# Performance work log

Hardware: AMD Instinct MI355X
Metric: run time of the kernel (lower is better)

## Reference

```python
import jax, jax.numpy as jnp
import numpy as np

WIN_LEN = 400
HOP = 100
NFFT = 512


def _make_kernel():
    # rfft of identity -> DFT basis, truncated to window length
    fb = np.fft.rfft(np.eye(NFFT))[:WIN_LEN]          # [WIN_LEN, NFFT//2+1] complex
    kernel = np.concatenate([fb.real, fb.imag], axis=1).T  # [2*(NFFT//2+1), WIN_LEN]
    # periodic (fftbins=True) Hamming window, as scipy.signal.get_window('hamming', N, fftbins=True)
    n = np.arange(WIN_LEN)
    window = (0.54 - 0.46 * np.cos(2.0 * np.pi * n / WIN_LEN)).astype(np.float32)
    kernel = kernel.astype(np.float32)[:, None, :] * window  # [514, 1, WIN_LEN]
    return jnp.asarray(kernel)


def setup_inputs() -> dict:
    key = jax.random.key(0)
    x = jax.random.normal(key, (32, 480000), dtype=jnp.float32)  # [B, T] raw audio
    return {"x": x, "weight": _make_kernel()}


def reference(x, weight):
    # x: [B, T] -> [B, 1, T]; pad both sides by (window_len - hop)
    pad = WIN_LEN - HOP
    xp = jnp.pad(x[:, None, :], ((0, 0), (0, 0), (pad, pad)))
    # strided conv against fixed Fourier basis -> [B, 2*(NFFT//2+1), n_frames]
    out = jax.lax.conv_general_dilated(
        xp, weight,
        window_strides=(HOP,),
        padding='VALID',
        dimension_numbers=('NCH', 'OIH', 'NCH'),
    )
    return out
```

## Files before the change

kernel.cpp:

```cpp
#include <hip/hip_runtime.h>
#include <hip/hip_bf16.h>


#define T_LEN   480000
#define NF      4803
#define C_OUT   514
#define HOP     100
#define WIN     400
#define BM      128
#define BN      64
#define WSTR    424
#define XPS     487040
#define XP_TOTAL (32 * XPS)
#define WP_ROWS 576
#define WP_ELEMS (WP_ROWS * WSTR)
#define WP_BYTE_OFF ((size_t)XP_TOTAL * 2)
#define WS_NEEDED (WP_BYTE_OFF + (size_t)WP_ELEMS * 2)
#define MT_CNT  38
#define NT_CNT  9
#define XSEG    13312

typedef __attribute__((ext_vector_type(8))) short short8;
typedef __attribute__((ext_vector_type(4))) float f32x4;

__device__ __forceinline__ unsigned short f2bf(float f) {
    unsigned int u = __float_as_uint(f);
    u += 0x7FFFu + ((u >> 16) & 1u);
    return (unsigned short)(u >> 16);
}

__device__ __forceinline__ void gl_lds16(const unsigned short* g, unsigned short* l) {
    __builtin_amdgcn_global_load_lds(
        (const __attribute__((address_space(1))) unsigned int*)(g),
        (__attribute__((address_space(3))) unsigned int*)(l), 16, 0, 0);
}

__global__ void cvt_x_kernel(const float* __restrict__ x, unsigned short* __restrict__ xp) {
    const int t = blockIdx.x * 256 + threadIdx.x;
    const int b  = t / (XPS / 4);
    const int i4 = t - b * (XPS / 4);
    const int i  = i4 * 4;
    const int g  = i - 300;
    ushort4 h;
    if (g >= 0 && g + 3 < T_LEN) {
        const float4 f = *(const float4*)(x + (size_t)b * T_LEN + g);
        h.x = f2bf(f.x); h.y = f2bf(f.y); h.z = f2bf(f.z); h.w = f2bf(f.w);
    } else {
        const float* xb = x + (size_t)b * T_LEN;
        h.x = (g + 0 >= 0 && g + 0 < T_LEN) ? f2bf(xb[g + 0]) : 0;
        h.y = (g + 1 >= 0 && g + 1 < T_LEN) ? f2bf(xb[g + 1]) : 0;
        h.z = (g + 2 >= 0 && g + 2 < T_LEN) ? f2bf(xb[g + 2]) : 0;
        h.w = (g + 3 >= 0 && g + 3 < T_LEN) ? f2bf(xb[g + 3]) : 0;
    }
    *(ushort4*)(xp + (size_t)b * XPS + i) = h;
}

__global__ void cvt_w_kernel(const float* __restrict__ w, unsigned short* __restrict__ wp) {
    const int t = blockIdx.x * 256 + threadIdx.x;
    if (t >= WP_ELEMS) return;
    const int c = t / WSTR;
    const int k = t - c * WSTR;
    wp[t] = (c < C_OUT && k < WIN) ? f2bf(w[(size_t)c * WIN + k]) : 0;
}

__global__ __launch_bounds__(256, 2)
void stft_gemm(const unsigned short* __restrict__ xp,
               const unsigned short* __restrict__ wp,
               float* __restrict__ out) {
    __shared__ unsigned short x_s[XSEG];
    __shared__ unsigned short w_s[BN * WSTR];

    const int tid  = threadIdx.x;
    const int lane = tid & 63;
    const int wv   = tid >> 6;
    const int nt   = blockIdx.x;
    const int mt   = blockIdx.y;
    const int b    = blockIdx.z;

    const unsigned short* xg = xp + (size_t)b * XPS + mt * (BM * HOP);
    #pragma unroll
    for (int c = wv; c < 26; c += 4) {
        const int idx = (c << 6) + lane;
        gl_lds16(xg + idx * 8, x_s + idx * 8);
    }
    const unsigned short* wg = wp + (size_t)nt * (BN * WSTR);
    #pragma unroll
    for (int c = wv; c < 53; c += 4) {
        const int idx = (c << 6) + lane;
        gl_lds16(wg + idx * 8, w_s + idx * 8);
    }
    __syncthreads();

    const int q  = lane >> 4;
    const int lm = lane & 15;

    f32x4 acc[2][4];
    #pragma unroll
    for (int mi = 0; mi < 2; ++mi)
        #pragma unroll
        for (int ni = 0; ni < 4; ++ni)
            acc[mi][ni] = (f32x4){0.f, 0.f, 0.f, 0.f};

    const int a0 = (wv * 32 + lm) * HOP + q * 8;
    const int a1 = a0 + 16 * HOP;
    int boff[4];
    #pragma unroll
    for (int ni = 0; ni < 4; ++ni) boff[ni] = (ni * 16 + lm) * WSTR + q * 8;

    #pragma unroll
    for (int kc = 0; kc < 13; ++kc) {
        const int k = kc * 32;
        union { short8 v; unsigned long long u[2]; } au0, au1;
        {
            const unsigned long long* p0 = (const unsigned long long*)(x_s + a0 + k);
            const unsigned long long* p1 = (const unsigned long long*)(x_s + a1 + k);
            au0.u[0] = p0[0]; au0.u[1] = p0[1];
            au1.u[0] = p1[0]; au1.u[1] = p1[1];
        }
        #pragma unroll
        for (int ni = 0; ni < 4; ++ni) {
            const short8 bf = *(const short8*)(&w_s[boff[ni] + k]);
            acc[0][ni] = __builtin_amdgcn_mfma_f32_16x16x32_bf16(au0.v, bf, acc[0][ni], 0, 0, 0);
            acc[1][ni] = __builtin_amdgcn_mfma_f32_16x16x32_bf16(au1.v, bf, acc[1][ni], 0, 0, 0);
        }
    }

    float* ob = out + (size_t)b * C_OUT * NF;
    const int f_base = mt * BM + wv * 32 + q * 4;
    const int c_base = nt * BN + lm;
    #pragma unroll
    for (int mi = 0; mi < 2; ++mi) {
        const int fg = f_base + mi * 16;
        const bool fok = (fg + 3 < NF);
        #pragma unroll
        for (int ni = 0; ni < 4; ++ni) {
            const int cg = c_base + ni * 16;
            if (cg < C_OUT) {
                float* op = ob + (size_t)cg * NF + fg;
                if (fok) {
                    op[0] = acc[mi][ni][0]; op[1] = acc[mi][ni][1];
                    op[2] = acc[mi][ni][2]; op[3] = acc[mi][ni][3];
                } else {
                    #pragma unroll
                    for (int r = 0; r < 4; ++r)
                        if (fg + r < NF) op[r] = acc[mi][ni][r];
                }
            }
        }
    }
}

#define SEG 13120
__global__ __launch_bounds__(256, 2)
void conv_stft_fallback(const float* __restrict__ x,
                        const float* __restrict__ w,
                        float* __restrict__ out) {
    __shared__ short x_s[SEG];
    __shared__ short w_s[BN * WSTR];
    const int tid = threadIdx.x;
    const int nt  = blockIdx.x;
    const int mt  = blockIdx.y;
    const int b   = blockIdx.z;
    const int s0 = mt * (BM * HOP) - 300;
    const float* xb = x + (size_t)b * T_LEN;
    for (int v = tid; v < SEG / 4; v += 256) {
        int g = s0 + v * 4;
        float f0, f1, f2, f3;
        if (g >= 0 && g + 3 < T_LEN) {
            const float4 f = *(const float4*)(xb + g);
            f0 = f.x; f1 = f.y; f2 = f.z; f3 = f.w;
        } else {
            f0 = (g + 0 >= 0 && g + 0 < T_LEN) ? xb[g + 0] : 0.f;
            f1 = (g + 1 >= 0 && g + 1 < T_LEN) ? xb[g + 1] : 0.f;
            f2 = (g + 2 >= 0 && g + 2 < T_LEN) ? xb[g + 2] : 0.f;
            f3 = (g + 3 >= 0 && g + 3 < T_LEN) ? xb[g + 3] : 0.f;
        }
        ushort4 h; h.x = f2bf(f0); h.y = f2bf(f1); h.z = f2bf(f2); h.w = f2bf(f3);
        *(ushort4*)(&x_s[v * 4]) = h;
    }
    for (int s = tid; s < BN * 106; s += 256) {
        const int r  = s / 106;
        const int gk = s - r * 106;
        const int c  = nt * BN + r;
        ushort4 h = make_ushort4(0, 0, 0, 0);
        if (gk < 100 && c < C_OUT) {
            const float4 f = *(const float4*)(w + (size_t)c * WIN + gk * 4);
            h.x = f2bf(f.x); h.y = f2bf(f.y); h.z = f2bf(f.z); h.w = f2bf(f.w);
        }
        if (gk * 4 < WSTR) *(ushort4*)(&w_s[r * WSTR + gk * 4]) = h;
    }
    __syncthreads();
    const int lane = tid & 63, wv = tid >> 6, q = lane >> 4, lm = lane & 15;
    f32x4 acc[2][4];
    #pragma unroll
    for (int mi = 0; mi < 2; ++mi)
        #pragma unroll
        for (int ni = 0; ni < 4; ++ni) acc[mi][ni] = (f32x4){0.f,0.f,0.f,0.f};
    const int a0 = (wv * 32 + lm) * HOP + q * 8;
    const int a1 = a0 + 16 * HOP;
    int boff[4];
    #pragma unroll
    for (int ni = 0; ni < 4; ++ni) boff[ni] = (ni * 16 + lm) * WSTR + q * 8;
    #pragma unroll
    for (int kc = 0; kc < 13; ++kc) {
        const int k = kc * 32;
        union { short8 v; unsigned long long u[2]; } au0, au1;
        const unsigned long long* p0 = (const unsigned long long*)(x_s + a0 + k);
        const unsigned long long* p1 = (const unsigned long long*)(x_s + a1 + k);
        au0.u[0] = p0[0]; au0.u[1] = p0[1];
        au1.u[0] = p1[0]; au1.u[1] = p1[1];
        #pragma unroll
        for (int ni = 0; ni < 4; ++ni) {
            const short8 bf = *(const short8*)(&w_s[boff[ni] + k]);
            acc[0][ni] = __builtin_amdgcn_mfma_f32_16x16x32_bf16(au0.v, bf, acc[0][ni], 0, 0, 0);
            acc[1][ni] = __builtin_amdgcn_mfma_f32_16x16x32_bf16(au1.v, bf, acc[1][ni], 0, 0, 0);
        }
    }
    float* ob = out + (size_t)b * C_OUT * NF;
    const int f_base = mt * BM + wv * 32 + q * 4;
    const int c_base = nt * BN + lm;
    #pragma unroll
    for (int mi = 0; mi < 2; ++mi) {
        #pragma unroll
        for (int ni = 0; ni < 4; ++ni) {
            const int cg = c_base + ni * 16;
            if (cg < C_OUT) {
                float* op = ob + (size_t)cg * NF;
                #pragma unroll
                for (int r = 0; r < 4; ++r) {
                    const int fg = f_base + mi * 16 + r;
                    if (fg < NF) op[fg] = acc[mi][ni][r];
                }
            }
        }
    }
}

extern "C" void kernel_launch(void* const* d_in, const int* in_sizes, int n_in,
                              void* d_out, int out_size, void* d_ws, size_t ws_size,
                              hipStream_t stream) {
    const float* x = (const float*)d_in[0];
    const float* w = (const float*)d_in[1];
    float* out = (float*)d_out;

    if (ws_size >= WS_NEEDED) {
        unsigned short* xp = (unsigned short*)d_ws;
        unsigned short* wp = (unsigned short*)((char*)d_ws + WP_BYTE_OFF);
        cvt_x_kernel<<<XP_TOTAL / 4 / 256, 256, 0, stream>>>(x, xp);
        cvt_w_kernel<<<(WP_ELEMS + 255) / 256, 256, 0, stream>>>(w, wp);
        dim3 grid(NT_CNT, MT_CNT, 32);
        stft_gemm<<<grid, 256, 0, stream>>>(xp, wp, out);
    } else {
        dim3 grid(NT_CNT, MT_CNT, 32);
        conv_stft_fallback<<<grid, 256, 0, stream>>>(x, w, out);
    }
}
```

Baseline: 455.9 us.

## Use 2-wave blocks with 4x4 MFMA tiles and XCD-aware block remapping

Halves the block to 128 threads, so each wave now computes a 64x64 output tile (4x4 MFMA fragments) instead of 32x64. This raises register-level reuse of A and B fragments read from LDS. The 3D grid is flattened to 1D and remapped so consecutive logical tiles land on the same XCD, aiming for better L2 locality of shared x and weight segments. The cost is more accumulator registers per thread and fewer waves per block to hide the global-to-LDS loads.

Measured after the change: 461.5 us. No clear change (+1.2%).

```diff
diff --git a/kernel.cpp b/kernel.cpp
--- a/kernel.cpp
+++ b/kernel.cpp
@@ -18,6 +18,8 @@
 #define WS_NEEDED (WP_BYTE_OFF + (size_t)WP_ELEMS * 2)
 #define MT_CNT  38
 #define NT_CNT  9
+#define TOT_BLK (NT_CNT * MT_CNT * 32)
+#define XCD_CHUNK (TOT_BLK / 8)
 #define XSEG    13312
 
 typedef __attribute__((ext_vector_type(8))) short short8;
@@ -63,7 +65,7 @@
     wp[t] = (c < C_OUT && k < WIN) ? f2bf(w[(size_t)c * WIN + k]) : 0;
 }
 
-__global__ __launch_bounds__(256, 2)
+__global__ __launch_bounds__(128, 2)
 void stft_gemm(const unsigned short* __restrict__ xp,
                const unsigned short* __restrict__ wp,
                float* __restrict__ out) {
@@ -73,19 +75,23 @@
     const int tid  = threadIdx.x;
     const int lane = tid & 63;
     const int wv   = tid >> 6;
-    const int nt   = blockIdx.x;
-    const int mt   = blockIdx.y;
-    const int b    = blockIdx.z;
+
+    const int id  = blockIdx.x;
+    const int lid = (id & 7) * XCD_CHUNK + (id >> 3);
+    const int nt  = lid % NT_CNT;
+    const int r1  = lid / NT_CNT;
+    const int mt  = r1 % MT_CNT;
+    const int b   = r1 / MT_CNT;
 
     const unsigned short* xg = xp + (size_t)b * XPS + mt * (BM * HOP);
     #pragma unroll
-    for (int c = wv; c < 26; c += 4) {
+    for (int c = wv; c < 26; c += 2) {
         const int idx = (c << 6) + lane;
         gl_lds16(xg + idx * 8, x_s + idx * 8);
     }
     const unsigned short* wg = wp + (size_t)nt * (BN * WSTR);
     #pragma unroll
-    for (int c = wv; c < 53; c += 4) {
+    for (int c = wv; c < 53; c += 2) {
         const int idx = (c << 6) + lane;
         gl_lds16(wg + idx * 8, w_s + idx * 8);
     }
@@ -94,15 +100,16 @@
     const int q  = lane >> 4;
     const int lm = lane & 15;
 
-    f32x4 acc[2][4];
-    #pragma unroll
-    for (int mi = 0; mi < 2; ++mi)
+    f32x4 acc[4][4];
+    #pragma unroll
+    for (int mi = 0; mi < 4; ++mi)
         #pragma unroll
         for (int ni = 0; ni < 4; ++ni)
             acc[mi][ni] = (f32x4){0.f, 0.f, 0.f, 0.f};
 
-    const int a0 = (wv * 32 + lm) * HOP + q * 8;
-    const int a1 = a0 + 16 * HOP;
+    int aoff[4];
+    #pragma unroll
+    for (int mi = 0; mi < 4; ++mi) aoff[mi] = (wv * 64 + mi * 16 + lm) * HOP + q * 8;
     int boff[4];
     #pragma unroll
     for (int ni = 0; ni < 4; ++ni) boff[ni] = (ni * 16 + lm) * WSTR + q * 8;
@@ -110,26 +117,26 @@
     #pragma unroll
     for (int kc = 0; kc < 13; ++kc) {
         const int k = kc * 32;
-        union { short8 v; unsigned long long u[2]; } au0, au1;
-        {
-            const unsigned long long* p0 = (const unsigned long long*)(x_s + a0 + k);
-            const unsigned long long* p1 = (const unsigned long long*)(x_s + a1 + k);
-            au0.u[0] = p0[0]; au0.u[1] = p0[1];
-            au1.u[0] = p1[0]; au1.u[1] = p1[1];
+        union { short8 v; unsigned long long u[2]; } au[4];
+        #pragma unroll
+        for (int mi = 0; mi < 4; ++mi) {
+            const unsigned long long* p = (const unsigned long long*)(x_s + aoff[mi] + k);
+            au[mi].u[0] = p[0]; au[mi].u[1] = p[1];
         }
         #pragma unroll
         for (int ni = 0; ni < 4; ++ni) {
             const short8 bf = *(const short8*)(&w_s[boff[ni] + k]);
-            acc[0][ni] = __builtin_amdgcn_mfma_f32_16x16x32_bf16(au0.v, bf, acc[0][ni], 0, 0, 0);
-            acc[1][ni] = __builtin_amdgcn_mfma_f32_16x16x32_bf16(au1.v, bf, acc[1][ni], 0, 0, 0);
+            #pragma unroll
+            for (int mi = 0; mi < 4; ++mi)
+                acc[mi][ni] = __builtin_amdgcn_mfma_f32_16x16x32_bf16(au[mi].v, bf, acc[mi][ni], 0, 0, 0);
         }
     }
 
     float* ob = out + (size_t)b * C_OUT * NF;
-    const int f_base = mt * BM + wv * 32 + q * 4;
+    const int f_base = mt * BM + wv * 64 + q * 4;
     const int c_base = nt * BN + lm;
     #pragma unroll
-    for (int mi = 0; mi < 2; ++mi) {
+    for (int mi = 0; mi < 4; ++mi) {
         const int fg = f_base + mi * 16;
         const bool fok = (fg + 3 < NF);
         #pragma unroll
@@ -248,8 +255,7 @@
         unsigned short* wp = (unsigned short*)((char*)d_ws + WP_BYTE_OFF);
         cvt_x_kernel<<<XP_TOTAL / 4 / 256, 256, 0, stream>>>(x, xp);
         cvt_w_kernel<<<(WP_ELEMS + 255) / 256, 256, 0, stream>>>(w, wp);
-        dim3 grid(NT_CNT, MT_CNT, 32);
-        stft_gemm<<<grid, 256, 0, stream>>>(xp, wp, out);
+        stft_gemm<<<dim3(TOT_BLK), 128, 0, stream>>>(xp, wp, out);
     } else {
         dim3 grid(NT_CNT, MT_CNT, 32);
         conv_stft_fallback<<<grid, 256, 0, stream>>>(x, w, out);
```

## Make STFT GEMM persistent with double-buffered input tiles and resident weights

Applied to the files above, without the earlier changes.

Replaces the one-block-per-tile grid with 256 persistent 512-thread blocks, each walking a contiguous range of tiles ordered so the weight tile stays resident in shared memory. The next audio segment is prefetched into a second LDS buffer while the current tile is computed, and weights reload only when the column tile changes. This aims to cut launch/tail overhead and redundant weight loads and to overlap loads with MFMA work, at the cost of lower occupancy (one block per CU) and a barrier per tile.

After: 467.5 us. 2.6% more time.

```diff
diff --git a/kernel.cpp b/kernel.cpp
--- a/kernel.cpp
+++ b/kernel.cpp
@@ -18,6 +18,8 @@
 #define WS_NEEDED (WP_BYTE_OFF + (size_t)WP_ELEMS * 2)
 #define MT_CNT  38
 #define NT_CNT  9
+#define NTILES  (NT_CNT * MT_CNT * 32)
+#define TPNT    (MT_CNT * 32)
 #define XSEG    13312
 
 typedef __attribute__((ext_vector_type(8))) short short8;
@@ -63,90 +65,136 @@
     wp[t] = (c < C_OUT && k < WIN) ? f2bf(w[(size_t)c * WIN + k]) : 0;
 }
 
-__global__ __launch_bounds__(256, 2)
+__device__ __forceinline__ void decode_tile(int t, int& nt, int& b, int& mt) {
+    nt = t / TPNT;
+    const int rem = t - nt * TPNT;
+    b  = rem / MT_CNT;
+    mt = rem - b * MT_CNT;
+}
+
+__global__ __launch_bounds__(512, 1)
 void stft_gemm(const unsigned short* __restrict__ xp,
                const unsigned short* __restrict__ wp,
                float* __restrict__ out) {
-    __shared__ unsigned short x_s[XSEG];
     __shared__ unsigned short w_s[BN * WSTR];
+    __shared__ unsigned short x_s[2][XSEG];
 
     const int tid  = threadIdx.x;
     const int lane = tid & 63;
     const int wv   = tid >> 6;
-    const int nt   = blockIdx.x;
-    const int mt   = blockIdx.y;
-    const int b    = blockIdx.z;
-
-    const unsigned short* xg = xp + (size_t)b * XPS + mt * (BM * HOP);
-    #pragma unroll
-    for (int c = wv; c < 26; c += 4) {
-        const int idx = (c << 6) + lane;
-        gl_lds16(xg + idx * 8, x_s + idx * 8);
-    }
-    const unsigned short* wg = wp + (size_t)nt * (BN * WSTR);
-    #pragma unroll
-    for (int c = wv; c < 53; c += 4) {
-        const int idx = (c << 6) + lane;
-        gl_lds16(wg + idx * 8, w_s + idx * 8);
+
+    const int id = blockIdx.x;
+    const int t0 = (id < 192) ? id * 43 : 192 * 43 + (id - 192) * 42;
+    const int nti = (id < 192) ? 43 : 42;
+
+    int nt, b, mt;
+    decode_tile(t0, nt, b, mt);
+
+    {
+        const unsigned short* wg = wp + (size_t)nt * (BN * WSTR);
+        #pragma unroll
+        for (int c = wv; c < 53; c += 8) {
+            const int idx = (c << 6) + lane;
+            gl_lds16(wg + idx * 8, w_s + idx * 8);
+        }
+        const unsigned short* xg = xp + (size_t)b * XPS + mt * (BM * HOP);
+        #pragma unroll
+        for (int c = wv; c < 26; c += 8) {
+            const int idx = (c << 6) + lane;
+            gl_lds16(xg + idx * 8, x_s[0] + idx * 8);
+        }
     }
     __syncthreads();
 
-    const int q  = lane >> 4;
+    const int q4 = lane >> 4;
     const int lm = lane & 15;
-
-    f32x4 acc[2][4];
-    #pragma unroll
-    for (int mi = 0; mi < 2; ++mi)
-        #pragma unroll
-        for (int ni = 0; ni < 4; ++ni)
-            acc[mi][ni] = (f32x4){0.f, 0.f, 0.f, 0.f};
-
-    const int a0 = (wv * 32 + lm) * HOP + q * 8;
-    const int a1 = a0 + 16 * HOP;
-    int boff[4];
-    #pragma unroll
-    for (int ni = 0; ni < 4; ++ni) boff[ni] = (ni * 16 + lm) * WSTR + q * 8;
-
-    #pragma unroll
-    for (int kc = 0; kc < 13; ++kc) {
-        const int k = kc * 32;
-        union { short8 v; unsigned long long u[2]; } au0, au1;
-        {
-            const unsigned long long* p0 = (const unsigned long long*)(x_s + a0 + k);
-            const unsigned long long* p1 = (const unsigned long long*)(x_s + a1 + k);
-            au0.u[0] = p0[0]; au0.u[1] = p0[1];
-            au1.u[0] = p1[0]; au1.u[1] = p1[1];
-        }
-        #pragma unroll
-        for (int ni = 0; ni < 4; ++ni) {
-            const short8 bf = *(const short8*)(&w_s[boff[ni] + k]);
-            acc[0][ni] = __builtin_amdgcn_mfma_f32_16x16x32_bf16(au0.v, bf, acc[0][ni], 0, 0, 0);
-            acc[1][ni] = __builtin_amdgcn_mfma_f32_16x16x32_bf16(au1.v, bf, acc[1][ni], 0, 0, 0);
-        }
-    }
-
-    float* ob = out + (size_t)b * C_OUT * NF;
-    const int f_base = mt * BM + wv * 32 + q * 4;
-    const int c_base = nt * BN + lm;
-    #pragma unroll
-    for (int mi = 0; mi < 2; ++mi) {
-        const int fg = f_base + mi * 16;
-        const bool fok = (fg + 3 < NF);
-        #pragma unroll
-        for (int ni = 0; ni < 4; ++ni) {
-            const int cg = c_base + ni * 16;
-            if (cg < C_OUT) {
-                float* op = ob + (size_t)cg * NF + fg;
-                if (fok) {
-                    op[0] = acc[mi][ni][0]; op[1] = acc[mi][ni][1];
-                    op[2] = acc[mi][ni][2]; op[3] = acc[mi][ni][3];
-                } else {
-                    #pragma unroll
-                    for (int r = 0; r < 4; ++r)
-                        if (fg + r < NF) op[r] = acc[mi][ni][r];
+    const int wr = wv & 3;
+    const int wc = wv >> 2;
+
+    int aoff[2];
+    #pragma unroll
+    for (int mi = 0; mi < 2; ++mi) aoff[mi] = (wr * 32 + mi * 16 + lm) * HOP + q4 * 8;
+    int boff[2];
+    #pragma unroll
+    for (int ni = 0; ni < 2; ++ni) boff[ni] = (wc * 32 + ni * 16 + lm) * WSTR + q4 * 8;
+
+    int cur = 0;
+    for (int ti = 0; ti < nti; ++ti) {
+        int nnt = nt, nb = 0, nmt = 0;
+        const bool have_next = (ti + 1 < nti);
+        if (have_next) {
+            decode_tile(t0 + ti + 1, nnt, nb, nmt);
+            const unsigned short* xg = xp + (size_t)nb * XPS + nmt * (BM * HOP);
+            unsigned short* xd = x_s[cur ^ 1];
+            #pragma unroll
+            for (int c = wv; c < 26; c += 8) {
+                const int idx = (c << 6) + lane;
+                gl_lds16(xg + idx * 8, xd + idx * 8);
+            }
+        }
+
+        const unsigned short* xs = x_s[cur];
+        f32x4 acc[2][2];
+        #pragma unroll
+        for (int mi = 0; mi < 2; ++mi)
+            #pragma unroll
+            for (int ni = 0; ni < 2; ++ni)
+                acc[mi][ni] = (f32x4){0.f, 0.f, 0.f, 0.f};
+
+        #pragma unroll
+        for (int kc = 0; kc < 13; ++kc) {
+            const int k = kc * 32;
+            union { short8 v; unsigned long long u[2]; } au[2];
+            #pragma unroll
+            for (int mi = 0; mi < 2; ++mi) {
+                const unsigned long long* p = (const unsigned long long*)(xs + aoff[mi] + k);
+                au[mi].u[0] = p[0]; au[mi].u[1] = p[1];
+            }
+            #pragma unroll
+            for (int ni = 0; ni < 2; ++ni) {
+                const short8 bf = *(const short8*)(&w_s[boff[ni] + k]);
+                #pragma unroll
+                for (int mi = 0; mi < 2; ++mi)
+                    acc[mi][ni] = __builtin_amdgcn_mfma_f32_16x16x32_bf16(au[mi].v, bf, acc[mi][ni], 0, 0, 0);
+            }
+        }
+
+        float* ob = out + (size_t)b * C_OUT * NF;
+        const int f_base = mt * BM + wr * 32 + q4 * 4;
+        const int c_base = nt * BN + wc * 32 + lm;
+        #pragma unroll
+        for (int mi = 0; mi < 2; ++mi) {
+            const int fg = f_base + mi * 16;
+            const bool fok = (fg + 3 < NF);
+            #pragma unroll
+            for (int ni = 0; ni < 2; ++ni) {
+                const int cg = c_base + ni * 16;
+                if (cg < C_OUT) {
+                    float* op = ob + (size_t)cg * NF + fg;
+                    if (fok) {
+                        op[0] = acc[mi][ni][0]; op[1] = acc[mi][ni][1];
+                        op[2] = acc[mi][ni][2]; op[3] = acc[mi][ni][3];
+                    } else {
+                        #pragma unroll
+                        for (int r = 0; r < 4; ++r)
+                            if (fg + r < NF) op[r] = acc[mi][ni][r];
+                    }
                 }
             }
         }
+
+        __syncthreads();
+        if (have_next && nnt != nt) {
+            const unsigned short* wg = wp + (size_t)nnt * (BN * WSTR);
+            #pragma unroll
+            for (int c = wv; c < 53; c += 8) {
+                const int idx = (c << 6) + lane;
+                gl_lds16(wg + idx * 8, w_s + idx * 8);
+            }
+            __syncthreads();
+        }
+        nt = nnt; b = nb; mt = nmt;
+        cur ^= 1;
     }
 }
 
@@ -248,8 +296,7 @@
         unsigned short* wp = (unsigned short*)((char*)d_ws + WP_BYTE_OFF);
         cvt_x_kernel<<<XP_TOTAL / 4 / 256, 256, 0, stream>>>(x, xp);
         cvt_w_kernel<<<(WP_ELEMS + 255) / 256, 256, 0, stream>>>(w, wp);
-        dim3 grid(NT_CNT, MT_CNT, 32);
-        stft_gemm<<<grid, 256, 0, stream>>>(xp, wp, out);
+        stft_gemm<<<dim3(256), 512, 0, stream>>>(xp, wp, out);
     } else {
         dim3 grid(NT_CNT, MT_CNT, 32);
         conv_stft_fallback<<<grid, 256, 0, stream>>>(x, w, out);
```
